# Kernel optimization log

Measured on AMD Instinct MI355X. Metric: run time of the kernel, lower is better.

## Reference

```python
import jax, jax.numpy as jnp
import numpy as np

PATCH = 16  # insize // num

def setup_inputs() -> dict:
    key = jax.random.key(0)
    k1, k2, k3 = jax.random.split(key, 3)
    B, C, H, W = 16, 2048, 64, 64
    P, Cr = 16, 128  # num*num patches, c // reduction
    x = jax.random.normal(k1, (B, C, H, W), dtype=jnp.float32)
    # stacked per-patch SE weights (Linear bias=False): fc1 [Cr, C], fc2 [C, Cr]
    W1 = jax.random.normal(k2, (P, Cr, C), dtype=jnp.float32) * (1.0 / np.sqrt(C))
    W2 = jax.random.normal(k3, (P, C, Cr), dtype=jnp.float32) * (1.0 / np.sqrt(Cr))
    return {"x": x, "W1": W1, "W2": W2}

def reference(x, W1, W2):
    # Faithful to original: every one of the P SE blocks pools the SAME
    # fixed patch x[..., ps:2ps, ps:2ps] (the loop indices are unused).
    ps = PATCH
    patch = x[..., ps:2 * ps, ps:2 * ps]          # [B, C, ps, ps]
    y = jnp.mean(patch, axis=(-2, -1))            # global avg pool -> [B, C]
    h = jax.nn.relu(jnp.einsum('pkc,bc->pbk', W1, y))   # [P, B, C/r]
    att = jax.nn.sigmoid(jnp.einsum('pck,pbk->pbc', W2, h))  # [P, B, C]
    return att[..., None, None]                   # [P, B, C, 1, 1] (stacked list)
```

## Files before the change

kernel.cpp:

```cpp
#include <hip/hip_runtime.h>
#include <math.h>

#define B_  16
#define C_  2048
#define H_  64
#define W_  64
#define P_  16
#define CR_ 128
#define PS_ 16

__global__ void k_mean(const float* __restrict__ x, float* __restrict__ y) {
    int wave = blockIdx.x * (blockDim.x >> 6) + (threadIdx.x >> 6);
    int lane = threadIdx.x & 63;
    int row = lane >> 2;
    int col = (lane & 3) * 4;
    const float* base = x + (size_t)wave * 4 * (H_ * W_) + PS_ * W_ + PS_
                      + row * W_ + col;
    float4 v0 = *reinterpret_cast<const float4*>(base);
    float4 v1 = *reinterpret_cast<const float4*>(base + H_ * W_);
    float4 v2 = *reinterpret_cast<const float4*>(base + 2 * H_ * W_);
    float4 v3 = *reinterpret_cast<const float4*>(base + 3 * H_ * W_);
    float s0 = v0.x + v0.y + v0.z + v0.w;
    float s1 = v1.x + v1.y + v1.z + v1.w;
    float s2 = v2.x + v2.y + v2.z + v2.w;
    float s3 = v3.x + v3.y + v3.z + v3.w;
    #pragma unroll
    for (int m = 32; m >= 1; m >>= 1) {
        s0 += __shfl_xor(s0, m, 64);
        s1 += __shfl_xor(s1, m, 64);
        s2 += __shfl_xor(s2, m, 64);
        s3 += __shfl_xor(s3, m, 64);
    }
    float v = s0;
    v = (lane == 1) ? s1 : v;
    v = (lane == 2) ? s2 : v;
    v = (lane == 3) ? s3 : v;
    if (lane < 4) y[wave * 4 + lane] = v * (1.0f / 256.0f);
}

__global__ void __launch_bounds__(256) k_fc1(const float* __restrict__ w1,
                                             const float* __restrict__ y,
                                             float* __restrict__ h) {
    __shared__ float ys[B_ * C_];
    int tid  = threadIdx.x;
    int wib  = tid >> 6;
    int lane = tid & 63;

    const float4* ysrc = reinterpret_cast<const float4*>(y);
    float4* ydst = reinterpret_cast<float4*>(ys);
    #pragma unroll 8
    for (int i = 0; i < 32; ++i)
        ydst[tid + 256 * i] = ysrc[tid + 256 * i];
    __syncthreads();

    int r0 = blockIdx.x * 8 + wib * 2;
    const float4* wr0 = reinterpret_cast<const float4*>(w1) + (size_t)r0 * (C_ / 4);
    const float4* wr1 = wr0 + (C_ / 4);

    float acc0[B_], acc1[B_];
    #pragma unroll
    for (int b = 0; b < B_; ++b) { acc0[b] = 0.0f; acc1[b] = 0.0f; }

    float4 pa = wr0[lane];
    float4 pb = wr1[lane];
    #pragma unroll
    for (int i = 0; i < 8; ++i) {
        float4 wa = pa, wb = pb;
        if (i < 7) { pa = wr0[(i + 1) * 64 + lane]; pb = wr1[(i + 1) * 64 + lane]; }
        const float4* yrow = reinterpret_cast<const float4*>(ys) + i * 64 + lane;
        #pragma unroll
        for (int b = 0; b < B_; ++b) {
            float4 v = yrow[b * (C_ / 4)];
            acc0[b] += wa.x * v.x + wa.y * v.y + wa.z * v.z + wa.w * v.w;
            acc1[b] += wb.x * v.x + wb.y * v.y + wb.z * v.z + wb.w * v.w;
        }
    }

    #pragma unroll
    for (int b = 0; b < B_; ++b) {
        #pragma unroll
        for (int m = 32; m >= 1; m >>= 1) {
            acc0[b] += __shfl_xor(acc0[b], m, 64);
            acc1[b] += __shfl_xor(acc1[b], m, 64);
        }
    }

    float v0 = acc0[0], v1 = acc1[0];
    #pragma unroll
    for (int b = 1; b < B_; ++b) {
        v0 = (lane == b) ? acc0[b] : v0;
        v1 = (lane == b) ? acc1[b] : v1;
    }
    if (lane < B_) {
        int p = r0 >> 7, k = r0 & 127;
        h[(p * B_ + lane) * CR_ + k]     = fmaxf(v0, 0.0f);
        h[(p * B_ + lane) * CR_ + k + 1] = fmaxf(v1, 0.0f);
    }
}

__global__ void __launch_bounds__(256) k_fc2(const float* __restrict__ w2,
                                             const float* __restrict__ h,
                                             float* __restrict__ out) {
    __shared__ float hs[B_ * CR_];

    int wib  = threadIdx.x >> 6;
    int wid  = blockIdx.x * 4 + wib;
    int lane = threadIdx.x & 63;
    int p  = wid >> 7;
    int c0 = (wid & 127) << 4;
    int row = lane >> 2;
    int q   = lane & 3;

    const float4* hsrc = reinterpret_cast<const float4*>(h + (size_t)p * B_ * CR_);
    float4* hdst = reinterpret_cast<float4*>(hs);
    #pragma unroll
    for (int i = 0; i < 2; ++i)
        hdst[threadIdx.x + i * 256] = hsrc[threadIdx.x + i * 256];
    __syncthreads();

    const float4* wr = reinterpret_cast<const float4*>(w2)
                     + ((size_t)p * C_ + c0 + row) * (CR_ / 4);
    const float4* hv = reinterpret_cast<const float4*>(hs);

    float acc[B_];
    #pragma unroll
    for (int b = 0; b < B_; ++b) acc[b] = 0.0f;

    #pragma unroll
    for (int j = 0; j < 8; ++j) {
        float4 w4 = wr[q + 4 * j];
        #pragma unroll
        for (int b = 0; b < B_; ++b) {
            float4 h4 = hv[b * (CR_ / 4) + q + 4 * j];
            acc[b] += w4.x * h4.x + w4.y * h4.y + w4.z * h4.z + w4.w * h4.w;
        }
    }

    #pragma unroll
    for (int b = 0; b < B_; ++b) {
        acc[b] += __shfl_xor(acc[b], 1, 64);
        acc[b] += __shfl_xor(acc[b], 2, 64);
    }

    #pragma unroll
    for (int i = 0; i < 4; ++i) {
        float v = acc[i];
        v = (q == 1) ? acc[4 + i]  : v;
        v = (q == 2) ? acc[8 + i]  : v;
        v = (q == 3) ? acc[12 + i] : v;
        int b = q * 4 + i;
        out[(((size_t)p * B_ + b) << 11) + c0 + row] = 1.0f / (1.0f + expf(-v));
    }
}

extern "C" void kernel_launch(void* const* d_in, const int* in_sizes, int n_in,
                              void* d_out, int out_size, void* d_ws, size_t ws_size,
                              hipStream_t stream) {
    const float* x  = (const float*)d_in[0];
    const float* w1 = (const float*)d_in[1];
    const float* w2 = (const float*)d_in[2];
    float* out = (float*)d_out;
    float* y = (float*)d_ws;
    float* h = y + B_ * C_;

    k_mean<<<(B_ * C_ / 4) / 4, 256, 0, stream>>>(x, y);
    k_fc1<<<256, 256, 0, stream>>>(w1, y, h);
    k_fc2<<<(P_ * C_ / 16) / 4, 256, 0, stream>>>(w2, h, out);
}
```

Measured before the change: 39.00 us.

## Fuse mean, fc1 and fc2 into one cooperative kernel with grid syncs

Replaces three kernel launches with a single cooperative kernel of 256 blocks by 512 threads that uses grid-wide syncs between the pooling, fc1 and fc2 stages. The aim is to remove per-launch overhead and inter-kernel gaps. The W1 rows are prefetched into registers before the fc1 stage, and y is staged through 64KB of shared memory in two passes. Half the waves sit idle during fc1, and the grid syncs add their own latency. The old three-kernel path is kept as a fallback if the cooperative launch fails.

```diff
diff --git a/kernel.cpp b/kernel.cpp
--- a/kernel.cpp
+++ b/kernel.cpp
@@ -1,100 +1,248 @@
 #include <hip/hip_runtime.h>
+#include <hip/hip_cooperative_groups.h>
 #include <math.h>
+
+namespace cg = cooperative_groups;
 
 #define B_  16
 #define C_  2048
-#define H_  64
-#define W_  64
 #define P_  16
 #define CR_ 128
-#define PS_ 16
+
+__global__ void __launch_bounds__(512, 2) k_fused(
+    const float* __restrict__ x, const float* __restrict__ w1,
+    const float* __restrict__ w2, float* __restrict__ out,
+    float* __restrict__ y, float* __restrict__ h)
+{
+    __shared__ float smem[16 * 1024];
+    float4* sm4 = reinterpret_cast<float4*>(smem);
+    const int tid  = threadIdx.x;
+    const int wib  = tid >> 6;
+    const int lane = tid & 63;
+    const int bid  = blockIdx.x;
+
+    {
+        const int wid = bid * 8 + wib;
+        const int row = lane >> 2, col = (lane & 3) * 4;
+        const float* base = x + (size_t)wid * 16 * 4096 + (16 * 64 + 16)
+                          + row * 64 + col;
+        #pragma unroll
+        for (int g = 0; g < 2; ++g) {
+            float s[8];
+            #pragma unroll
+            for (int j = 0; j < 8; ++j) {
+                float4 v = *reinterpret_cast<const float4*>(base + (g * 8 + j) * 4096);
+                s[j] = (v.x + v.y) + (v.z + v.w);
+            }
+            #pragma unroll
+            for (int j = 0; j < 8; ++j) {
+                #pragma unroll
+                for (int m = 32; m >= 1; m >>= 1) s[j] += __shfl_xor(s[j], m, 64);
+            }
+            float v = s[0];
+            v = (lane == 1) ? s[1] : v;
+            v = (lane == 2) ? s[2] : v;
+            v = (lane == 3) ? s[3] : v;
+            v = (lane == 4) ? s[4] : v;
+            v = (lane == 5) ? s[5] : v;
+            v = (lane == 6) ? s[6] : v;
+            v = (lane == 7) ? s[7] : v;
+            if (lane < 8) y[wid * 16 + g * 8 + lane] = v * (1.0f / 256.0f);
+        }
+    }
+
+    cg::this_grid().sync();
+
+    {
+        const float4* yv  = reinterpret_cast<const float4*>(y);
+        const float4* w1v = reinterpret_cast<const float4*>(w1);
+        const bool work = (wib < 4);
+        const int r0 = (bid * 4 + wib) * 2;
+
+        float4 wA[8], wB[8];
+        if (work) {
+            #pragma unroll
+            for (int i = 0; i < 8; ++i) {
+                wA[i] = w1v[(size_t)r0 * 512 + i * 64 + lane];
+                wB[i] = w1v[(size_t)(r0 + 1) * 512 + i * 64 + lane];
+            }
+        }
+        float acc0[16], acc1[16];
+        #pragma unroll
+        for (int b = 0; b < 16; ++b) { acc0[b] = 0.f; acc1[b] = 0.f; }
+
+        #pragma unroll
+        for (int pass = 0; pass < 2; ++pass) {
+            #pragma unroll
+            for (int i = 0; i < 8; ++i) {
+                int f = i * 512 + tid;
+                int b = f >> 8, c4 = f & 255;
+                sm4[f] = yv[b * 512 + pass * 256 + c4];
+            }
+            __syncthreads();
+            if (work) {
+                #pragma unroll
+                for (int il = 0; il < 4; ++il) {
+                    float4 wa = wA[pass * 4 + il];
+                    float4 wb = wB[pass * 4 + il];
+                    #pragma unroll
+                    for (int b = 0; b < 16; ++b) {
+                        float4 v = sm4[b * 256 + il * 64 + lane];
+                        acc0[b] += wa.x * v.x + wa.y * v.y + wa.z * v.z + wa.w * v.w;
+                        acc1[b] += wb.x * v.x + wb.y * v.y + wb.z * v.z + wb.w * v.w;
+                    }
+                }
+            }
+            __syncthreads();
+        }
+
+        if (work) {
+            #pragma unroll
+            for (int b = 0; b < 16; ++b) {
+                #pragma unroll
+                for (int m = 32; m >= 1; m >>= 1) {
+                    acc0[b] += __shfl_xor(acc0[b], m, 64);
+                    acc1[b] += __shfl_xor(acc1[b], m, 64);
+                }
+            }
+            float v0 = acc0[0], v1 = acc1[0];
+            #pragma unroll
+            for (int b = 1; b < 16; ++b) {
+                v0 = (lane == b) ? acc0[b] : v0;
+                v1 = (lane == b) ? acc1[b] : v1;
+            }
+            if (lane < 16) {
+                const int p = r0 >> 7, k = r0 & 127;
+                h[(p * B_ + lane) * CR_ + k]     = fmaxf(v0, 0.f);
+                h[(p * B_ + lane) * CR_ + k + 1] = fmaxf(v1, 0.f);
+            }
+        }
+    }
+
+    cg::this_grid().sync();
+
+    {
+        const int p   = bid >> 4;
+        const int c0  = (bid & 15) * 128 + wib * 16;
+        const int row = lane >> 2, q = lane & 3;
+
+        const float4* hv = reinterpret_cast<const float4*>(h);
+        sm4[tid] = hv[p * 512 + tid];
+        __syncthreads();
+
+        const float4* wr = reinterpret_cast<const float4*>(w2)
+                         + ((size_t)p * C_ + c0 + row) * (CR_ / 4);
+        float4 wv[8];
+        #pragma unroll
+        for (int j = 0; j < 8; ++j) wv[j] = wr[q + 4 * j];
+
+        float acc[16];
+        #pragma unroll
+        for (int b = 0; b < 16; ++b) acc[b] = 0.f;
+        #pragma unroll
+        for (int j = 0; j < 8; ++j) {
+            #pragma unroll
+            for (int b = 0; b < 16; ++b) {
+                float4 h4 = sm4[b * 32 + q + 4 * j];
+                acc[b] += wv[j].x * h4.x + wv[j].y * h4.y
+                        + wv[j].z * h4.z + wv[j].w * h4.w;
+            }
+        }
+        #pragma unroll
+        for (int b = 0; b < 16; ++b) {
+            acc[b] += __shfl_xor(acc[b], 1, 64);
+            acc[b] += __shfl_xor(acc[b], 2, 64);
+        }
+        #pragma unroll
+        for (int i = 0; i < 4; ++i) {
+            float v = acc[i];
+            v = (q == 1) ? acc[4 + i]  : v;
+            v = (q == 2) ? acc[8 + i]  : v;
+            v = (q == 3) ? acc[12 + i] : v;
+            int b = q * 4 + i;
+            out[(((size_t)p * B_ + b) << 11) + c0 + row] = 1.0f / (1.0f + expf(-v));
+        }
+    }
+}
 
 __global__ void k_mean(const float* __restrict__ x, float* __restrict__ y) {
     int wave = blockIdx.x * (blockDim.x >> 6) + (threadIdx.x >> 6);
     int lane = threadIdx.x & 63;
-    int row = lane >> 2;
-    int col = (lane & 3) * 4;
-    const float* base = x + (size_t)wave * 4 * (H_ * W_) + PS_ * W_ + PS_
-                      + row * W_ + col;
+    int row = lane >> 2, col = (lane & 3) * 4;
+    const float* base = x + (size_t)wave * 4 * 4096 + (16 * 64 + 16) + row * 64 + col;
     float4 v0 = *reinterpret_cast<const float4*>(base);
-    float4 v1 = *reinterpret_cast<const float4*>(base + H_ * W_);
-    float4 v2 = *reinterpret_cast<const float4*>(base + 2 * H_ * W_);
-    float4 v3 = *reinterpret_cast<const float4*>(base + 3 * H_ * W_);
+    float4 v1 = *reinterpret_cast<const float4*>(base + 4096);
+    float4 v2 = *reinterpret_cast<const float4*>(base + 8192);
+    float4 v3 = *reinterpret_cast<const float4*>(base + 12288);
     float s0 = v0.x + v0.y + v0.z + v0.w;
     float s1 = v1.x + v1.y + v1.z + v1.w;
     float s2 = v2.x + v2.y + v2.z + v2.w;
     float s3 = v3.x + v3.y + v3.z + v3.w;
     #pragma unroll
     for (int m = 32; m >= 1; m >>= 1) {
-        s0 += __shfl_xor(s0, m, 64);
-        s1 += __shfl_xor(s1, m, 64);
-        s2 += __shfl_xor(s2, m, 64);
-        s3 += __shfl_xor(s3, m, 64);
+        s0 += __shfl_xor(s0, m, 64); s1 += __shfl_xor(s1, m, 64);
+        s2 += __shfl_xor(s2, m, 64); s3 += __shfl_xor(s3, m, 64);
     }
     float v = s0;
-    v = (lane == 1) ? s1 : v;
-    v = (lane == 2) ? s2 : v;
-    v = (lane == 3) ? s3 : v;
+    v = (lane == 1) ? s1 : v; v = (lane == 2) ? s2 : v; v = (lane == 3) ? s3 : v;
     if (lane < 4) y[wave * 4 + lane] = v * (1.0f / 256.0f);
 }
 
 __global__ void __launch_bounds__(256) k_fc1(const float* __restrict__ w1,
                                              const float* __restrict__ y,
                                              float* __restrict__ h) {
-    __shared__ float ys[B_ * C_];
-    int tid  = threadIdx.x;
-    int wib  = tid >> 6;
-    int lane = tid & 63;
-
-    const float4* ysrc = reinterpret_cast<const float4*>(y);
-    float4* ydst = reinterpret_cast<float4*>(ys);
-    #pragma unroll 8
-    for (int i = 0; i < 32; ++i)
-        ydst[tid + 256 * i] = ysrc[tid + 256 * i];
-    __syncthreads();
-
+    __shared__ float ys[B_ * C_ / 2];
+    int tid = threadIdx.x, wib = tid >> 6, lane = tid & 63;
+    const float4* yv = reinterpret_cast<const float4*>(y);
+    float4* sm4 = reinterpret_cast<float4*>(ys);
     int r0 = blockIdx.x * 8 + wib * 2;
-    const float4* wr0 = reinterpret_cast<const float4*>(w1) + (size_t)r0 * (C_ / 4);
-    const float4* wr1 = wr0 + (C_ / 4);
-
-    float acc0[B_], acc1[B_];
-    #pragma unroll
-    for (int b = 0; b < B_; ++b) { acc0[b] = 0.0f; acc1[b] = 0.0f; }
-
-    float4 pa = wr0[lane];
-    float4 pb = wr1[lane];
-    #pragma unroll
-    for (int i = 0; i < 8; ++i) {
-        float4 wa = pa, wb = pb;
-        if (i < 7) { pa = wr0[(i + 1) * 64 + lane]; pb = wr1[(i + 1) * 64 + lane]; }
-        const float4* yrow = reinterpret_cast<const float4*>(ys) + i * 64 + lane;
-        #pragma unroll
-        for (int b = 0; b < B_; ++b) {
-            float4 v = yrow[b * (C_ / 4)];
-            acc0[b] += wa.x * v.x + wa.y * v.y + wa.z * v.z + wa.w * v.w;
-            acc1[b] += wb.x * v.x + wb.y * v.y + wb.z * v.z + wb.w * v.w;
-        }
-    }
-
-    #pragma unroll
-    for (int b = 0; b < B_; ++b) {
+    const float4* wr0 = reinterpret_cast<const float4*>(w1) + (size_t)r0 * 512;
+    const float4* wr1 = wr0 + 512;
+    float4 wA[8], wB[8];
+    #pragma unroll
+    for (int i = 0; i < 8; ++i) { wA[i] = wr0[i * 64 + lane]; wB[i] = wr1[i * 64 + lane]; }
+    float acc0[16], acc1[16];
+    #pragma unroll
+    for (int b = 0; b < 16; ++b) { acc0[b] = 0.f; acc1[b] = 0.f; }
+    #pragma unroll
+    for (int pass = 0; pass < 2; ++pass) {
+        #pragma unroll
+        for (int i = 0; i < 16; ++i) {
+            int f = i * 256 + tid;
+            int b = f >> 8, c4 = f & 255;
+            sm4[f] = yv[b * 512 + pass * 256 + c4];
+        }
+        __syncthreads();
+        #pragma unroll
+        for (int il = 0; il < 4; ++il) {
+            float4 wa = wA[pass * 4 + il], wb = wB[pass * 4 + il];
+            #pragma unroll
+            for (int b = 0; b < 16; ++b) {
+                float4 v = sm4[b * 256 + il * 64 + lane];
+                acc0[b] += wa.x * v.x + wa.y * v.y + wa.z * v.z + wa.w * v.w;
+                acc1[b] += wb.x * v.x + wb.y * v.y + wb.z * v.z + wb.w * v.w;
+            }
+        }
+        __syncthreads();
+    }
+    #pragma unroll
+    for (int b = 0; b < 16; ++b) {
         #pragma unroll
         for (int m = 32; m >= 1; m >>= 1) {
             acc0[b] += __shfl_xor(acc0[b], m, 64);
             acc1[b] += __shfl_xor(acc1[b], m, 64);
         }
     }
-
     float v0 = acc0[0], v1 = acc1[0];
     #pragma unroll
-    for (int b = 1; b < B_; ++b) {
+    for (int b = 1; b < 16; ++b) {
         v0 = (lane == b) ? acc0[b] : v0;
         v1 = (lane == b) ? acc1[b] : v1;
     }
-    if (lane < B_) {
+    if (lane < 16) {
         int p = r0 >> 7, k = r0 & 127;
-        h[(p * B_ + lane) * CR_ + k]     = fmaxf(v0, 0.0f);
-        h[(p * B_ + lane) * CR_ + k + 1] = fmaxf(v1, 0.0f);
+        h[(p * B_ + lane) * CR_ + k]     = fmaxf(v0, 0.f);
+        h[(p * B_ + lane) * CR_ + k + 1] = fmaxf(v1, 0.f);
     }
 }
 
@@ -102,51 +250,41 @@
                                              const float* __restrict__ h,
                                              float* __restrict__ out) {
     __shared__ float hs[B_ * CR_];
-
-    int wib  = threadIdx.x >> 6;
-    int wid  = blockIdx.x * 4 + wib;
+    int wib = threadIdx.x >> 6;
+    int wid = blockIdx.x * 4 + wib;
     int lane = threadIdx.x & 63;
-    int p  = wid >> 7;
-    int c0 = (wid & 127) << 4;
-    int row = lane >> 2;
-    int q   = lane & 3;
-
+    int p = wid >> 7, c0 = (wid & 127) << 4;
+    int row = lane >> 2, q = lane & 3;
     const float4* hsrc = reinterpret_cast<const float4*>(h + (size_t)p * B_ * CR_);
     float4* hdst = reinterpret_cast<float4*>(hs);
     #pragma unroll
-    for (int i = 0; i < 2; ++i)
-        hdst[threadIdx.x + i * 256] = hsrc[threadIdx.x + i * 256];
+    for (int i = 0; i < 2; ++i) hdst[threadIdx.x + i * 256] = hsrc[threadIdx.x + i * 256];
     __syncthreads();
-
     const float4* wr = reinterpret_cast<const float4*>(w2)
                      + ((size_t)p * C_ + c0 + row) * (CR_ / 4);
     const float4* hv = reinterpret_cast<const float4*>(hs);
-
-    float acc[B_];
-    #pragma unroll
-    for (int b = 0; b < B_; ++b) acc[b] = 0.0f;
-
+    float acc[16];
+    #pragma unroll
+    for (int b = 0; b < 16; ++b) acc[b] = 0.f;
     #pragma unroll
     for (int j = 0; j < 8; ++j) {
         float4 w4 = wr[q + 4 * j];
         #pragma unroll
-        for (int b = 0; b < B_; ++b) {
-            float4 h4 = hv[b * (CR_ / 4) + q + 4 * j];
+        for (int b = 0; b < 16; ++b) {
+            float4 h4 = hv[b * 32 + q + 4 * j];
             acc[b] += w4.x * h4.x + w4.y * h4.y + w4.z * h4.z + w4.w * h4.w;
         }
     }
-
-    #pragma unroll
-    for (int b = 0; b < B_; ++b) {
+    #pragma unroll
+    for (int b = 0; b < 16; ++b) {
         acc[b] += __shfl_xor(acc[b], 1, 64);
         acc[b] += __shfl_xor(acc[b], 2, 64);
     }
-
     #pragma unroll
     for (int i = 0; i < 4; ++i) {
         float v = acc[i];
-        v = (q == 1) ? acc[4 + i]  : v;
-        v = (q == 2) ? acc[8 + i]  : v;
+        v = (q == 1) ? acc[4 + i] : v;
+        v = (q == 2) ? acc[8 + i] : v;
         v = (q == 3) ? acc[12 + i] : v;
         int b = q * 4 + i;
         out[(((size_t)p * B_ + b) << 11) + c0 + row] = 1.0f / (1.0f + expf(-v));
@@ -163,7 +301,14 @@
     float* y = (float*)d_ws;
     float* h = y + B_ * C_;
 
-    k_mean<<<(B_ * C_ / 4) / 4, 256, 0, stream>>>(x, y);
-    k_fc1<<<256, 256, 0, stream>>>(w1, y, h);
-    k_fc2<<<(P_ * C_ / 16) / 4, 256, 0, stream>>>(w2, h, out);
-}
+    void* args[] = { (void*)&x, (void*)&w1, (void*)&w2, (void*)&out,
+                     (void*)&y, (void*)&h };
+    hipError_t err = hipLaunchCooperativeKernel((const void*)k_fused,
+                                                dim3(256), dim3(512),
+                                                args, 0, stream);
+    if (err != hipSuccess) {
+        k_mean<<<(B_ * C_ / 4) / 4, 256, 0, stream>>>(x, y);
+        k_fc1<<<256, 256, 0, stream>>>(w1, y, h);
+        k_fc2<<<(P_ * C_ / 16) / 4, 256, 0, stream>>>(w2, h, out);
+    }
+}
```

After: 103.5 us. +165.4%, slower.
